# Kernel tuning notes

Measured on AMD Instinct MI355X. Metric: run time of the kernel, lower is better.

The kernel has to match this reference:

```python
import jax, jax.numpy as jnp
import numpy as np

N_NODES = 100000
N_EDGES = 1600000
IN_DIM = 128
HIDDEN = 128


def setup_inputs() -> dict:
    key = jax.random.key(0)
    k1, k2, k3, k4 = jax.random.split(key, 4)
    x = jax.random.normal(k1, (N_NODES, IN_DIM), dtype=jnp.float32)
    edge_index = jax.random.randint(k2, (2, N_EDGES), 0, N_NODES, dtype=jnp.int32)
    # Glorot-ish scale (module zero-inits weights, which would give trivial
    # outputs; use random weights for a meaningful correctness baseline).
    W1 = jax.random.normal(k3, (IN_DIM, HIDDEN), dtype=jnp.float32) * (1.0 / np.sqrt(IN_DIM))
    W2 = jax.random.normal(k4, (HIDDEN, HIDDEN), dtype=jnp.float32) * (1.0 / np.sqrt(HIDDEN))
    return {"x": x, "edge_index": edge_index, "W1": W1, "W2": W2}


def _gcn_conv(h, W, src, dst, norm):
    # linear transform then normalized scatter-add aggregation (PyG GCNConv, bias=False)
    h = h @ W                              # [N, H]
    msg = h[src] * norm[:, None]           # gather + scale: [E+N, H]
    return jax.ops.segment_sum(msg, dst, num_segments=N_NODES)


def reference(x, edge_index, W1, W2):
    # add self-loops
    loops = jnp.arange(N_NODES, dtype=edge_index.dtype)
    src = jnp.concatenate([edge_index[0], loops])
    dst = jnp.concatenate([edge_index[1], loops])
    # symmetric normalization D^{-1/2} (A+I) D^{-1/2}; deg >= 1 due to self-loops
    deg = jax.ops.segment_sum(jnp.ones_like(dst, dtype=x.dtype), dst, num_segments=N_NODES)
    dinv = jax.lax.rsqrt(deg)
    norm = dinv[src] * dinv[dst]           # [E+N]

    h = _gcn_conv(x, W1, src, dst, norm)
    h = jax.nn.relu(h)                     # dropout is identity in eval mode
    h = _gcn_conv(h, W2, src, dst, norm)
    return h
```

## Files before the change

### kernel.cpp

```cpp
#include <hip/hip_runtime.h>
#include <hip/hip_bf16.h>

typedef unsigned short u16;
typedef unsigned int   u32;

typedef __attribute__((ext_vector_type(8))) short short8;
typedef __attribute__((ext_vector_type(4))) float floatx4;

#define HD __device__ __forceinline__

HD float bf16_lo(u32 u) { union { u32 i; float f; } v; v.i = u << 16; return v.f; }
HD float bf16_hi(u32 u) { union { u32 i; float f; } v; v.i = u & 0xffff0000u; return v.f; }
HD u16 f2bf(float f) {
    __hip_bfloat16 h = __float2bfloat16(f);
    u16 s; __builtin_memcpy(&s, &h, 2); return s;
}

#define NPB   256
#define MAXNB 512
#define CH    4096

__global__ void k_detect(const u32* __restrict__ xw, int* __restrict__ flag) {
    __shared__ int cnt;
    if (threadIdx.x == 0) cnt = 0;
    __syncthreads();
    int sane = 0;
    for (int i = threadIdx.x; i < 4096; i += 256) {
        u32 v = xw[i];
        int e = (v >> 7) & 0xFF;
        sane += (e >= 107 && e <= 147) ? 1 : 0;
    }
    atomicAdd(&cnt, sane);
    __syncthreads();
    if (threadIdx.x == 0) *flag = (cnt > 2048) ? 1 : 0;
}

__global__ void k_bhist(const int* __restrict__ dst, int* __restrict__ gbcnt, int E) {
    __shared__ int h[MAXNB];
    for (int i = threadIdx.x; i < MAXNB; i += 256) h[i] = 0;
    __syncthreads();
    int base = blockIdx.x * CH;
    int end  = min(base + CH, E);
    for (int i = base + threadIdx.x; i < end; i += 256)
        atomicAdd(&h[dst[i] >> 8], 1);
    __syncthreads();
    for (int i = threadIdx.x; i < MAXNB; i += 256)
        if (h[i]) atomicAdd(&gbcnt[i], h[i]);
}

__global__ void k_bscan(const int* __restrict__ gbcnt, int* __restrict__ gboff,
                        int* __restrict__ gbcursor, int NB) {
    int lane = threadIdx.x;
    int carry = 0;
    int T = (NB + 63) / 64;
    for (int t = 0; t < T; t++) {
        int i = t * 64 + lane;
        int v = (i < NB) ? gbcnt[i] : 0;
        int x = v;
#pragma unroll
        for (int off = 1; off < 64; off <<= 1) {
            int y = __shfl_up(x, off);
            if (lane >= off) x += y;
        }
        if (i < NB) { int ex = carry + x - v; gboff[i] = ex; gbcursor[i] = ex; }
        carry += __shfl(x, 63);
    }
    if (lane == 0) gboff[NB] = carry;
}

__global__ void __launch_bounds__(256)
k_coarse(const int* __restrict__ ei, int* __restrict__ gbcursor,
         int2* __restrict__ pairs, int E) {
    __shared__ int  hist[MAXNB];
    __shared__ int  gs[MAXNB];
    __shared__ int  dlt[MAXNB];
    __shared__ int  lofs[MAXNB];
    __shared__ int2 lp[CH];
    __shared__ u16  pb[CH];
    const int* srcp = ei;
    const int* dstp = ei + E;
    int base = blockIdx.x * CH;
    int cnt  = min(CH, E - base);

    for (int i = threadIdx.x; i < MAXNB; i += 256) hist[i] = 0;
    __syncthreads();

    int2 e[16];
    int nb_ = 0;
#pragma unroll
    for (int j = 0; j < 16; j++) {
        int i = base + threadIdx.x + j * 256;
        if (i < E) {
            e[j].x = srcp[i];
            e[j].y = dstp[i];
            atomicAdd(&hist[e[j].y >> 8], 1);
            nb_ = j + 1;
        }
    }
    __syncthreads();

    if (threadIdx.x < 64) {
        int lane = threadIdx.x;
        int carry = 0;
#pragma unroll
        for (int t = 0; t < MAXNB / 64; t++) {
            int i = t * 64 + lane;
            int v = hist[i];
            int x = v;
#pragma unroll
            for (int off = 1; off < 64; off <<= 1) {
                int y = __shfl_up(x, off);
                if (lane >= off) x += y;
            }
            gs[i] = carry + x - v;
            carry += __shfl(x, 63);
        }
    }
    __syncthreads();

    for (int b = threadIdx.x; b < MAXNB; b += 256) {
        int c = hist[b];
        lofs[b] = gs[b];
        if (c > 0) {
            int gbase = atomicAdd(&gbcursor[b], c);
            dlt[b] = gbase - gs[b];
        }
    }
    __syncthreads();

    for (int j = 0; j < nb_; j++) {
        int b = e[j].y >> 8;
        int p = atomicAdd(&lofs[b], 1);
        lp[p] = e[j];
        pb[p] = (u16)b;
    }
    __syncthreads();

    for (int p = threadIdx.x; p < cnt; p += 256) {
        pairs[p + dlt[pb[p]]] = lp[p];
    }
}

__global__ void k_nodecnt(const int2* __restrict__ pairs, const int* __restrict__ gboff,
                          int* __restrict__ cnt, int N) {
    __shared__ int lc[NPB];
    int b = blockIdx.x;
    int nbase = b * NPB;
    lc[threadIdx.x] = 0;
    __syncthreads();
    int p0 = gboff[b], p1 = gboff[b + 1];
    for (int p = p0 + threadIdx.x; p < p1; p += 256)
        atomicAdd(&lc[pairs[p].y - nbase], 1);
    __syncthreads();
    int node = nbase + threadIdx.x;
    if (node < N) cnt[node] = lc[threadIdx.x];
}

__global__ void k_fine(const int2* __restrict__ pairs, const int* __restrict__ gboff,
                       const int* __restrict__ rowptr, int* __restrict__ col, int N) {
    __shared__ int lcur[NPB];
    int b = blockIdx.x;
    int nbase = b * NPB;
    int node = nbase + threadIdx.x;
    lcur[threadIdx.x] = (node < N) ? rowptr[node] : 0;
    __syncthreads();
    int p0 = gboff[b], p1 = gboff[b + 1];
    for (int p = p0 + threadIdx.x; p < p1; p += 256) {
        int2 e = pairs[p];
        int pos = atomicAdd(&lcur[e.y - nbase], 1);
        col[pos] = e.x;
    }
}

__global__ void k_dinv(const int* __restrict__ cnt, float* __restrict__ dinv, int N) {
    int i = blockIdx.x * blockDim.x + threadIdx.x;
    if (i < N) dinv[i] = rsqrtf((float)cnt[i] + 1.0f);
}

__global__ void k_blocksum(const int* __restrict__ cnt, int* __restrict__ partial, int N) {
    __shared__ int wsum[4];
    int base = blockIdx.x * 1024;
    int s = 0;
#pragma unroll
    for (int j = 0; j < 4; j++) {
        int i = base + j * 256 + threadIdx.x;
        if (i < N) s += cnt[i];
    }
#pragma unroll
    for (int off = 32; off > 0; off >>= 1) s += __shfl_down(s, off);
    if ((threadIdx.x & 63) == 0) wsum[threadIdx.x >> 6] = s;
    __syncthreads();
    if (threadIdx.x == 0) partial[blockIdx.x] = wsum[0] + wsum[1] + wsum[2] + wsum[3];
}

__global__ void k_scanpart(int* __restrict__ partial, int* __restrict__ rowptrN, int P) {
    int lane = threadIdx.x;
    int carry = 0;
    int T = (P + 63) / 64;
    for (int t = 0; t < T; t++) {
        int i = t * 64 + lane;
        int v = (i < P) ? partial[i] : 0;
        int x = v;
#pragma unroll
        for (int off = 1; off < 64; off <<= 1) {
            int y = __shfl_up(x, off);
            if (lane >= off) x += y;
        }
        if (i < P) partial[i] = carry + x - v;
        carry += __shfl(x, 63);
    }
    if (lane == 0) *rowptrN = carry;
}

__global__ void __launch_bounds__(1024)
k_scanfinal(const int* __restrict__ cnt, const int* __restrict__ partial,
            int* __restrict__ rowptr, int* __restrict__ cursor, int N) {
    __shared__ int ws[16];
    int lane = threadIdx.x & 63, wid = threadIdx.x >> 6;
    int i = blockIdx.x * 1024 + threadIdx.x;
    int v = (i < N) ? cnt[i] : 0;
    int x = v;
#pragma unroll
    for (int off = 1; off < 64; off <<= 1) {
        int y = __shfl_up(x, off);
        if (lane >= off) x += y;
    }
    if (lane == 63) ws[wid] = x;
    __syncthreads();
    if (wid == 0) {
        int w = (lane < 16) ? ws[lane] : 0;
        int wx = w;
#pragma unroll
        for (int off = 1; off < 16; off <<= 1) {
            int y = __shfl_up(wx, off);
            if (lane >= off) wx += y;
        }
        if (lane < 16) ws[lane] = wx - w;
    }
    __syncthreads();
    int excl = partial[blockIdx.x] + ws[wid] + (x - v);
    if (i < N) { rowptr[i] = excl; cursor[i] = excl; }
}

__global__ void k_transpose(const void* __restrict__ W1, const void* __restrict__ W2,
                            u16* __restrict__ W1t, u16* __restrict__ W2t,
                            const int* __restrict__ flagp) {
    int isbf = *flagp;
    int i = blockIdx.x * blockDim.x + threadIdx.x;
    int w = i >> 14;
    int r = (i >> 7) & 127;
    int c = i & 127;
    const void* W = w ? W2 : W1;
    u16*       Wt = w ? W2t : W1t;
    u16 val;
    if (isbf) val = ((const u16*)W)[c * 128 + r];
    else      val = f2bf(((const float*)W)[c * 128 + r]);
    Wt[r * 128 + c] = val;
}

template <int MODE>
__global__ void __launch_bounds__(256)
k_gemm(const void* __restrict__ inp, const u16* __restrict__ Wt,
       u16* __restrict__ outb, int ntiles, const int* __restrict__ flagp) {
    __shared__ u16 lw[128 * 128];
    __shared__ u16 stage[4][16 * 136];
    int isbf = (MODE == 0) ? *flagp : 1;
    int gw   = (blockIdx.x * blockDim.x + threadIdx.x) >> 6;
    int nw   = (gridDim.x * blockDim.x) >> 6;
    int lane = threadIdx.x & 63;
    int wid  = threadIdx.x >> 6;
    int m = lane & 15, q = lane >> 4;
    u16* st = stage[wid];

    {
        int r = threadIdx.x >> 1;
        int h = threadIdx.x & 1;
        const short8* src = (const short8*)(Wt + r * 128 + h * 64);
#pragma unroll
        for (int jj = 0; jj < 8; jj++) {
            int slot = h * 8 + jj;
            *(short8*)&lw[r * 128 + ((slot ^ (r & 7)) << 3)] = src[jj];
        }
    }
    __syncthreads();

    for (int t = gw; t < ntiles; t += nw) {
        long r0 = (long)t * 32;
        floatx4 acc[2][8];
#pragma unroll
        for (int g = 0; g < 2; g++)
#pragma unroll
            for (int nt = 0; nt < 8; nt++) acc[g][nt] = (floatx4)0.0f;

        short8 a[2][4];
        if (MODE == 1 || isbf) {
#pragma unroll
            for (int g = 0; g < 2; g++)
#pragma unroll
                for (int kk = 0; kk < 4; kk++)
                    a[g][kk] = *(const short8*)((const u16*)inp +
                                 (r0 + g * 16 + m) * 128 + kk * 32 + q * 8);
        } else {
#pragma unroll
            for (int g = 0; g < 2; g++)
#pragma unroll
                for (int kk = 0; kk < 4; kk++) {
                    const float4* fp = (const float4*)((const float*)inp +
                                 (r0 + g * 16 + m) * 128 + kk * 32 + q * 8);
                    float4 f0 = fp[0], f1 = fp[1];
                    short8 v;
                    v[0] = (short)f2bf(f0.x); v[1] = (short)f2bf(f0.y);
                    v[2] = (short)f2bf(f0.z); v[3] = (short)f2bf(f0.w);
                    v[4] = (short)f2bf(f1.x); v[5] = (short)f2bf(f1.y);
                    v[6] = (short)f2bf(f1.z); v[7] = (short)f2bf(f1.w);
                    a[g][kk] = v;
                }
        }

#pragma unroll
        for (int kk = 0; kk < 4; kk++) {
#pragma unroll
            for (int nt = 0; nt < 8; nt++) {
                int slot = kk * 4 + q;
                short8 b = *(const short8*)&lw[(nt * 16 + m) * 128 +
                                               ((slot ^ (m & 7)) << 3)];
                acc[0][nt] = __builtin_amdgcn_mfma_f32_16x16x32_bf16(a[0][kk], b, acc[0][nt], 0, 0, 0);
                acc[1][nt] = __builtin_amdgcn_mfma_f32_16x16x32_bf16(a[1][kk], b, acc[1][nt], 0, 0, 0);
            }
        }

#pragma unroll
        for (int g = 0; g < 2; g++) {
#pragma unroll
            for (int nt = 0; nt < 8; nt++)
#pragma unroll
                for (int i = 0; i < 4; i++)
                    st[(q * 4 + i) * 136 + nt * 16 + m] = f2bf(acc[g][nt][i]);
            __builtin_amdgcn_s_waitcnt(0);
            u16* gbase = outb + (size_t)(r0 + g * 16) * 128;
#pragma unroll
            for (int j = 0; j < 4; j++) {
                int e   = lane * 8 + j * 512;
                int row = e >> 7, colu = e & 127;
                short8 vv = *(const short8*)&st[row * 136 + colu];
                *(short8*)(gbase + e) = vv;
            }
            __builtin_amdgcn_s_waitcnt(0);
        }
    }
}

template <int MODE>
__global__ void k_csr_agg(const u16* __restrict__ Hb, const int* __restrict__ col,
                          const int* __restrict__ rowptr, const float* __restrict__ dinv,
                          void* __restrict__ outp, int N, const int* __restrict__ flagp) {
    int isbf = MODE ? *flagp : 1;
    int gw   = (blockIdx.x * blockDim.x + threadIdx.x) >> 6;
    int nw   = (gridDim.x * blockDim.x) >> 6;
    int lane = threadIdx.x & 63;
    for (int n = gw; n < N; n += nw) {
        int r0 = rowptr[n], r1 = rowptr[n + 1];
        float di = dinv[n];
        u32 h = *(const u32*)(Hb + (size_t)n * 128 + lane * 2);
        float c = di * di;
        float a0 = bf16_lo(h) * c, a1 = bf16_hi(h) * c;

        for (int base = r0; base < r1; base += 64) {
            int cnt = min(64, r1 - base);
            int   myc = (lane < cnt) ? col[base + lane] : 0;
            float mdv = (lane < cnt) ? dinv[myc] : 0.0f;
            int e = 0;
            for (; e + 7 < cnt; e += 8) {
                u32 hh[8]; float cf[8];
#pragma unroll
                for (int j = 0; j < 8; j++) {
                    int   s = __shfl(myc, e + j);
                    cf[j]   = __shfl(mdv, e + j) * di;
                    hh[j]   = *(const u32*)(Hb + (size_t)s * 128 + lane * 2);
                }
#pragma unroll
                for (int j = 0; j < 8; j++) {
                    a0 += bf16_lo(hh[j]) * cf[j];
                    a1 += bf16_hi(hh[j]) * cf[j];
                }
            }
            for (; e + 3 < cnt; e += 4) {
                u32 hh[4]; float cf[4];
#pragma unroll
                for (int j = 0; j < 4; j++) {
                    int   s = __shfl(myc, e + j);
                    cf[j]   = __shfl(mdv, e + j) * di;
                    hh[j]   = *(const u32*)(Hb + (size_t)s * 128 + lane * 2);
                }
#pragma unroll
                for (int j = 0; j < 4; j++) {
                    a0 += bf16_lo(hh[j]) * cf[j];
                    a1 += bf16_hi(hh[j]) * cf[j];
                }
            }
            for (; e < cnt; e++) {
                int   s  = __shfl(myc, e);
                float cf = __shfl(mdv, e) * di;
                u32  hh  = *(const u32*)(Hb + (size_t)s * 128 + lane * 2);
                a0 += bf16_lo(hh) * cf; a1 += bf16_hi(hh) * cf;
            }
        }

        if (MODE == 0) {
            float r0f = fmaxf(a0, 0.0f), r1f = fmaxf(a1, 0.0f);
            ((u32*)outp)[(size_t)n * 64 + lane] = (u32)f2bf(r0f) | ((u32)f2bf(r1f) << 16);
        } else if (isbf) {
            ((u32*)outp)[(size_t)n * 64 + lane] = (u32)f2bf(a0) | ((u32)f2bf(a1) << 16);
        } else {
            ((float2*)outp)[(size_t)n * 64 + lane] = make_float2(a0, a1);
        }
    }
}

extern "C" void kernel_launch(void* const* d_in, const int* in_sizes, int n_in,
                              void* d_out, int out_size, void* d_ws, size_t ws_size,
                              hipStream_t stream) {
    const void* x  = d_in[0];
    const int*  ei = (const int*)d_in[1];
    const void* W1 = d_in[2];
    const void* W2 = d_in[3];

    const int N = in_sizes[0] / 128;
    const int E = in_sizes[1] / 2;

    char* ws = (char*)d_ws;
    float* dinv    = (float*)ws;
    int*   cnt     = (int*)(ws + (512u << 10));
    int*   rowptr  = (int*)(ws + (1024u << 10));
    int*   partial = (int*)(ws + (1536u << 10));
    int*   gbcnt   = (int*)(ws + (1600u << 10));
    int*   gboff   = (int*)(ws + (1664u << 10));
    int*   gbcur   = (int*)(ws + (1728u << 10));
    int*   flag    = (int*)(ws + (1984u << 10));
    u16*   W1t     = (u16*)(ws + (2048u << 10));
    u16*   W2t     = W1t + 128 * 128;
    int*   col     = (int*)(ws + (3u << 20));
    u16*   Hb      = (u16*)(ws + (10u << 20));
    u16*   A       = (u16*)(ws + (40u << 20));
    int2*  pairs   = (int2*)(ws + (70u << 20));

    int P   = (N + 1023) / 1024;
    int NB  = (N + NPB - 1) / NPB;
    int nch = (E + CH - 1) / CH;

    k_detect<<<1, 256, 0, stream>>>((const u32*)x, flag);
    hipMemsetAsync(gbcnt, 0, (size_t)(MAXNB + 1) * 4, stream);
    k_bhist<<<nch, 256, 0, stream>>>(ei + E, gbcnt, E);
    k_bscan<<<1, 64, 0, stream>>>(gbcnt, gboff, gbcur, NB);
    k_coarse<<<nch, 256, 0, stream>>>(ei, gbcur, pairs, E);
    k_nodecnt<<<NB, 256, 0, stream>>>(pairs, gboff, cnt, N);
    k_dinv<<<(N + 255) / 256, 256, 0, stream>>>(cnt, dinv, N);
    k_blocksum<<<P, 256, 0, stream>>>(cnt, partial, N);
    k_scanpart<<<1, 64, 0, stream>>>(partial, rowptr + N, P);
    k_scanfinal<<<P, 1024, 0, stream>>>(cnt, partial, rowptr, cnt , N);
    k_fine<<<NB, 256, 0, stream>>>(pairs, gboff, rowptr, col, N);
    k_transpose<<<128, 256, 0, stream>>>(W1, W2, W1t, W2t, flag);

    int ntiles  = N / 32;
    int gblocks = (ntiles + 3) / 4;
    int ablocks = (N + 3) / 4;

    k_gemm<0><<<gblocks, 256, 0, stream>>>(x, W1t, Hb, ntiles, flag);
    k_csr_agg<0><<<ablocks, 256, 0, stream>>>(Hb, col, rowptr, dinv, A, N, flag);

    k_gemm<1><<<gblocks, 256, 0, stream>>>(A, W2t, Hb, ntiles, flag);
    k_csr_agg<1><<<ablocks, 256, 0, stream>>>(Hb, col, rowptr, dinv, d_out, N, flag);
}
```

Before: 344.6 us.

## Fuse CSR build passes into one bucket kernel and merge weight prep

Merges node counting, degree normalisation, prefix scan and column fill into one per-bucket kernel that takes row offsets from the bucket offsets instead of a global scan. Also folds dtype detection, the histogram memset and the weight transpose into one kernel, and adds a 16-wide unrolled gather loop in aggregation. The goal is to cut about eight kernel launches and their serial dependencies. The cost is redundant detection work in every block and higher register pressure from the wider unroll.

```diff
diff --git a/kernel.cpp b/kernel.cpp
--- a/kernel.cpp
+++ b/kernel.cpp
@@ -20,7 +20,10 @@
 #define MAXNB 512
 #define CH    4096
 
-__global__ void k_detect(const u32* __restrict__ xw, int* __restrict__ flag) {
+__global__ void k_wprep(const u32* __restrict__ xw,
+                        const void* __restrict__ W1, const void* __restrict__ W2,
+                        u16* __restrict__ W1t, u16* __restrict__ W2t,
+                        int* __restrict__ flag, int* __restrict__ gbcnt) {
     __shared__ int cnt;
     if (threadIdx.x == 0) cnt = 0;
     __syncthreads();
@@ -32,7 +35,21 @@
     }
     atomicAdd(&cnt, sane);
     __syncthreads();
-    if (threadIdx.x == 0) *flag = (cnt > 2048) ? 1 : 0;
+    int isbf = (cnt > 2048) ? 1 : 0;
+    if (blockIdx.x == 0) {
+        if (threadIdx.x == 0) *flag = isbf;
+        for (int i = threadIdx.x; i <= MAXNB; i += 256) gbcnt[i] = 0;
+    }
+    int i = blockIdx.x * blockDim.x + threadIdx.x;
+    int w = i >> 14;
+    int r = (i >> 7) & 127;
+    int c = i & 127;
+    const void* W = w ? W2 : W1;
+    u16*       Wt = w ? W2t : W1t;
+    u16 val;
+    if (isbf) val = ((const u16*)W)[c * 128 + r];
+    else      val = f2bf(((const float*)W)[c * 128 + r]);
+    Wt[r * 128 + c] = val;
 }
 
 __global__ void k_bhist(const int* __restrict__ dst, int* __restrict__ gbcnt, int E) {
@@ -141,121 +158,50 @@
     }
 }
 
-__global__ void k_nodecnt(const int2* __restrict__ pairs, const int* __restrict__ gboff,
-                          int* __restrict__ cnt, int N) {
+__global__ void __launch_bounds__(256)
+k_bucket(const int2* __restrict__ pairs, const int* __restrict__ gboff,
+         float* __restrict__ dinv, int* __restrict__ rowptr,
+         int* __restrict__ col, int N, int E) {
     __shared__ int lc[NPB];
+    __shared__ int lcur[NPB];
+    __shared__ int ws[4];
+    __shared__ int wsoff[4];
     int b = blockIdx.x;
     int nbase = b * NPB;
-    lc[threadIdx.x] = 0;
+    int tid = threadIdx.x, lane = tid & 63, wid = tid >> 6;
+    lc[tid] = 0;
     __syncthreads();
     int p0 = gboff[b], p1 = gboff[b + 1];
-    for (int p = p0 + threadIdx.x; p < p1; p += 256)
+    for (int p = p0 + tid; p < p1; p += 256)
         atomicAdd(&lc[pairs[p].y - nbase], 1);
     __syncthreads();
-    int node = nbase + threadIdx.x;
-    if (node < N) cnt[node] = lc[threadIdx.x];
-}
-
-__global__ void k_fine(const int2* __restrict__ pairs, const int* __restrict__ gboff,
-                       const int* __restrict__ rowptr, int* __restrict__ col, int N) {
-    __shared__ int lcur[NPB];
-    int b = blockIdx.x;
-    int nbase = b * NPB;
-    int node = nbase + threadIdx.x;
-    lcur[threadIdx.x] = (node < N) ? rowptr[node] : 0;
-    __syncthreads();
-    int p0 = gboff[b], p1 = gboff[b + 1];
-    for (int p = p0 + threadIdx.x; p < p1; p += 256) {
+    int v = lc[tid];
+    int node = nbase + tid;
+    if (node < N) dinv[node] = rsqrtf((float)v + 1.0f);
+    int x = v;
+#pragma unroll
+    for (int off = 1; off < 64; off <<= 1) {
+        int y = __shfl_up(x, off);
+        if (lane >= off) x += y;
+    }
+    if (lane == 63) ws[wid] = x;
+    __syncthreads();
+    if (tid == 0) {
+        int s = 0;
+#pragma unroll
+        for (int k2 = 0; k2 < 4; k2++) { wsoff[k2] = s; s += ws[k2]; }
+    }
+    __syncthreads();
+    int excl = p0 + wsoff[wid] + (x - v);
+    if (node < N) rowptr[node] = excl;
+    lcur[tid] = excl;
+    if (b == 0 && tid == 0) rowptr[N] = E;
+    __syncthreads();
+    for (int p = p0 + tid; p < p1; p += 256) {
         int2 e = pairs[p];
         int pos = atomicAdd(&lcur[e.y - nbase], 1);
         col[pos] = e.x;
     }
-}
-
-__global__ void k_dinv(const int* __restrict__ cnt, float* __restrict__ dinv, int N) {
-    int i = blockIdx.x * blockDim.x + threadIdx.x;
-    if (i < N) dinv[i] = rsqrtf((float)cnt[i] + 1.0f);
-}
-
-__global__ void k_blocksum(const int* __restrict__ cnt, int* __restrict__ partial, int N) {
-    __shared__ int wsum[4];
-    int base = blockIdx.x * 1024;
-    int s = 0;
-#pragma unroll
-    for (int j = 0; j < 4; j++) {
-        int i = base + j * 256 + threadIdx.x;
-        if (i < N) s += cnt[i];
-    }
-#pragma unroll
-    for (int off = 32; off > 0; off >>= 1) s += __shfl_down(s, off);
-    if ((threadIdx.x & 63) == 0) wsum[threadIdx.x >> 6] = s;
-    __syncthreads();
-    if (threadIdx.x == 0) partial[blockIdx.x] = wsum[0] + wsum[1] + wsum[2] + wsum[3];
-}
-
-__global__ void k_scanpart(int* __restrict__ partial, int* __restrict__ rowptrN, int P) {
-    int lane = threadIdx.x;
-    int carry = 0;
-    int T = (P + 63) / 64;
-    for (int t = 0; t < T; t++) {
-        int i = t * 64 + lane;
-        int v = (i < P) ? partial[i] : 0;
-        int x = v;
-#pragma unroll
-        for (int off = 1; off < 64; off <<= 1) {
-            int y = __shfl_up(x, off);
-            if (lane >= off) x += y;
-        }
-        if (i < P) partial[i] = carry + x - v;
-        carry += __shfl(x, 63);
-    }
-    if (lane == 0) *rowptrN = carry;
-}
-
-__global__ void __launch_bounds__(1024)
-k_scanfinal(const int* __restrict__ cnt, const int* __restrict__ partial,
-            int* __restrict__ rowptr, int* __restrict__ cursor, int N) {
-    __shared__ int ws[16];
-    int lane = threadIdx.x & 63, wid = threadIdx.x >> 6;
-    int i = blockIdx.x * 1024 + threadIdx.x;
-    int v = (i < N) ? cnt[i] : 0;
-    int x = v;
-#pragma unroll
-    for (int off = 1; off < 64; off <<= 1) {
-        int y = __shfl_up(x, off);
-        if (lane >= off) x += y;
-    }
-    if (lane == 63) ws[wid] = x;
-    __syncthreads();
-    if (wid == 0) {
-        int w = (lane < 16) ? ws[lane] : 0;
-        int wx = w;
-#pragma unroll
-        for (int off = 1; off < 16; off <<= 1) {
-            int y = __shfl_up(wx, off);
-            if (lane >= off) wx += y;
-        }
-        if (lane < 16) ws[lane] = wx - w;
-    }
-    __syncthreads();
-    int excl = partial[blockIdx.x] + ws[wid] + (x - v);
-    if (i < N) { rowptr[i] = excl; cursor[i] = excl; }
-}
-
-__global__ void k_transpose(const void* __restrict__ W1, const void* __restrict__ W2,
-                            u16* __restrict__ W1t, u16* __restrict__ W2t,
-                            const int* __restrict__ flagp) {
-    int isbf = *flagp;
-    int i = blockIdx.x * blockDim.x + threadIdx.x;
-    int w = i >> 14;
-    int r = (i >> 7) & 127;
-    int c = i & 127;
-    const void* W = w ? W2 : W1;
-    u16*       Wt = w ? W2t : W1t;
-    u16 val;
-    if (isbf) val = ((const u16*)W)[c * 128 + r];
-    else      val = f2bf(((const float*)W)[c * 128 + r]);
-    Wt[r * 128 + c] = val;
 }
 
 template <int MODE>
@@ -370,6 +316,20 @@
             int   myc = (lane < cnt) ? col[base + lane] : 0;
             float mdv = (lane < cnt) ? dinv[myc] : 0.0f;
             int e = 0;
+            for (; e + 15 < cnt; e += 16) {
+                u32 hh[16]; float cf[16];
+#pragma unroll
+                for (int j = 0; j < 16; j++) {
+                    int   s = __shfl(myc, e + j);
+                    cf[j]   = __shfl(mdv, e + j) * di;
+                    hh[j]   = *(const u32*)(Hb + (size_t)s * 128 + lane * 2);
+                }
+#pragma unroll
+                for (int j = 0; j < 16; j++) {
+                    a0 += bf16_lo(hh[j]) * cf[j];
+                    a1 += bf16_hi(hh[j]) * cf[j];
+                }
+            }
             for (; e + 7 < cnt; e += 8) {
                 u32 hh[8]; float cf[8];
 #pragma unroll
@@ -430,9 +390,7 @@
 
     char* ws = (char*)d_ws;
     float* dinv    = (float*)ws;
-    int*   cnt     = (int*)(ws + (512u << 10));
     int*   rowptr  = (int*)(ws + (1024u << 10));
-    int*   partial = (int*)(ws + (1536u << 10));
     int*   gbcnt   = (int*)(ws + (1600u << 10));
     int*   gboff   = (int*)(ws + (1664u << 10));
     int*   gbcur   = (int*)(ws + (1728u << 10));
@@ -444,22 +402,14 @@
     u16*   A       = (u16*)(ws + (40u << 20));
     int2*  pairs   = (int2*)(ws + (70u << 20));
 
-    int P   = (N + 1023) / 1024;
     int NB  = (N + NPB - 1) / NPB;
     int nch = (E + CH - 1) / CH;
 
-    k_detect<<<1, 256, 0, stream>>>((const u32*)x, flag);
-    hipMemsetAsync(gbcnt, 0, (size_t)(MAXNB + 1) * 4, stream);
+    k_wprep<<<128, 256, 0, stream>>>((const u32*)x, W1, W2, W1t, W2t, flag, gbcnt);
     k_bhist<<<nch, 256, 0, stream>>>(ei + E, gbcnt, E);
     k_bscan<<<1, 64, 0, stream>>>(gbcnt, gboff, gbcur, NB);
     k_coarse<<<nch, 256, 0, stream>>>(ei, gbcur, pairs, E);
-    k_nodecnt<<<NB, 256, 0, stream>>>(pairs, gboff, cnt, N);
-    k_dinv<<<(N + 255) / 256, 256, 0, stream>>>(cnt, dinv, N);
-    k_blocksum<<<P, 256, 0, stream>>>(cnt, partial, N);
-    k_scanpart<<<1, 64, 0, stream>>>(partial, rowptr + N, P);
-    k_scanfinal<<<P, 1024, 0, stream>>>(cnt, partial, rowptr, cnt , N);
-    k_fine<<<NB, 256, 0, stream>>>(pairs, gboff, rowptr, col, N);
-    k_transpose<<<128, 256, 0, stream>>>(W1, W2, W1t, W2t, flag);
+    k_bucket<<<NB, 256, 0, stream>>>(pairs, gboff, dinv, rowptr, col, N, E);
 
     int ntiles  = N / 32;
     int gblocks = (ntiles + 3) / 4;
```

Result: faster. 327.5 us (-5.0%).
